# Performance work log

Measured on AMD Instinct MI355X. Metric: run time of the kernel, lower is better.

The kernel has to match this reference:

```python
import jax, jax.numpy as jnp
import numpy as np

HIDDEN = 64
NUM_LAYERS = 6
BN_EPS = 1e-5


def setup_inputs() -> dict:
    key = jax.random.key(0)
    N, M = 1024, 1024
    num_nodes = N + M
    ks = jax.random.split(key, 12)
    x = jax.random.normal(ks[0], (num_nodes, 2), dtype=jnp.float32)
    # complete bipartite edges: (a, N+b) for all a in [0,N), b in [0,M), row-major so view(N,M) is meaningful
    row = jnp.repeat(jnp.arange(N, dtype=jnp.int64), M)
    col = N + jnp.tile(jnp.arange(M, dtype=jnp.int64), N)
    edge_index = jnp.stack([row, col], axis=0)
    s = 1.0 / np.sqrt(HIDDEN)
    return {
        "x": x,
        "edge_index": edge_index,
        "in_w": jax.random.normal(ks[1], (2, HIDDEN), jnp.float32) * 0.5,
        "in_b": jnp.zeros((HIDDEN,), jnp.float32),
        "conv_w": jax.random.normal(ks[2], (NUM_LAYERS, HIDDEN, HIDDEN), jnp.float32) * s,
        "conv_b": jnp.zeros((NUM_LAYERS, HIDDEN), jnp.float32),
        "bn_gamma": jnp.ones((NUM_LAYERS, HIDDEN), jnp.float32),
        "bn_beta": jnp.zeros((NUM_LAYERS, HIDDEN), jnp.float32),
        "out_w": jax.random.normal(ks[3], (2 * HIDDEN, 1), jnp.float32) * s,
        "out_b": jnp.zeros((1,), jnp.float32),
        "N": N,
        "M": M,
    }


def reference(x, edge_index, in_w, in_b, conv_w, conv_b, bn_gamma, bn_beta, out_w, out_b, N, M):
    num_nodes = x.shape[0]
    # GCN normalization with added self-loops (PyG GCNConv defaults)
    loops = jnp.arange(num_nodes, dtype=edge_index.dtype)
    row = jnp.concatenate([edge_index[0], loops])
    col = jnp.concatenate([edge_index[1], loops])
    deg = jax.ops.segment_sum(jnp.ones_like(col, dtype=x.dtype), col, num_segments=num_nodes)
    dinv = jnp.where(deg > 0, jax.lax.rsqrt(deg), 0.0)
    norm = dinv[row] * dinv[col]  # [E+num_nodes]

    h = jax.nn.relu(x @ in_w + in_b)
    for i in range(NUM_LAYERS):
        h_res = h
        hw = h @ conv_w[i]
        agg = jax.ops.segment_sum(hw[row] * norm[:, None], col, num_segments=num_nodes)
        h = agg + conv_b[i]
        # BatchNorm1d in training mode: batch stats, biased variance
        mu = h.mean(axis=0)
        var = ((h - mu) ** 2).mean(axis=0)
        h = (h - mu) * jax.lax.rsqrt(var + BN_EPS) * bn_gamma[i] + bn_beta[i]
        h = jax.nn.relu(h)
        if i > 0 and i % 2 == 1:
            h = h + h_res

    ef = jnp.concatenate([h[edge_index[0]], h[edge_index[1]]], axis=1)  # [E, 2H]
    scores = (ef @ out_w + out_b)[:, 0]
    return scores.reshape(N, M)
```

## Files before the change

kernel.cpp:

```cpp
#include <hip/hip_runtime.h>


#define NBLK 64
#define MAGIC 0x13572468u

__device__ __forceinline__ float relu_(float x) { return x > 0.f ? x : 0.f; }

#define AT_LOAD(p)    __hip_atomic_load((p), __ATOMIC_RELAXED, __HIP_MEMORY_SCOPE_AGENT)
#define AT_STORE(p,v) __hip_atomic_store((p), (v), __ATOMIC_RELAXED, __HIP_MEMORY_SCOPE_AGENT)
#define AT_ADD(p,v)   __hip_atomic_fetch_add((p), (v), __ATOMIC_RELAXED, __HIP_MEMORY_SCOPE_AGENT)

#define PART_OFF  256
#define UV_OFF    12544
#define FLAG_OFF  14592

__global__ __launch_bounds__(256, 1) void k_fused(
    const float* __restrict__ x,
    const float* __restrict__ in_w, const float* __restrict__ in_b,
    const float* __restrict__ conv_w,
    const float* __restrict__ bn_g, const float* __restrict__ bn_b,
    const float* __restrict__ out_w,
    unsigned int* __restrict__ ws)
{
    __shared__ float Wl[2][4096];
    __shared__ float hl[32 * 68];
    __shared__ float sredS[4 * 64], sredQ[4 * 64];
    __shared__ float stat[256];
    __shared__ float pcoef[64], scoef[64];
    __shared__ float g_lds[384], b_lds[384];
    __shared__ float ow_lds[128];

    const int t = threadIdx.x, b = blockIdx.x;
    const int nl = t >> 3;
    const int fi = t & 7;
    const int f0 = fi * 8;
    const int node = b * 32 + nl;
    const bool isA = b < 32;
    float* part = (float*)(ws + PART_OFF);
    float* uv   = (float*)(ws + UV_OFF);

    {
        const float4* src = (const float4*)conv_w;
        float4* dst = (float4*)Wl[0];
        dst[t]       = src[t];
        dst[t + 256] = src[t + 256];
        dst[t + 512] = src[t + 512];
        dst[t + 768] = src[t + 768];
        for (int i = t; i < 384; i += 256) { g_lds[i] = bn_g[i]; b_lds[i] = bn_b[i]; }
        if (t < 128) ow_lds[t] = out_w[t];
    }

    if (b == 0) {
        for (int i = t; i < 192; i += 256) AT_STORE(ws + i, 0u);
        for (int i = t; i < 12288; i += 256) AT_STORE((unsigned*)part + i, 0u);
        asm volatile("s_waitcnt vmcnt(0)" ::: "memory");
        __syncthreads();
        if (t == 0) AT_STORE(ws + FLAG_OFF, MAGIC);
    }

    {
        float x0 = x[node * 2], x1 = x[node * 2 + 1];
#pragma unroll
        for (int j = 0; j < 8; j++) {
            int f = f0 + j;
            hl[nl * 68 + f] = relu_(fmaf(x0, in_w[f], fmaf(x1, in_w[64 + f], in_b[f])));
        }
    }
    __syncthreads();

    for (int layer = 0; layer < 6; layer++) {
        const float* Wb = Wl[layer & 1];
        float acc[8];
#pragma unroll
        for (int j = 0; j < 8; j++) acc[j] = 0.f;

#pragma unroll 4
        for (int k = 0; k < 64; k += 4) {
            float4 hh = *(const float4*)&hl[nl * 68 + k];
            float hv[4] = {hh.x, hh.y, hh.z, hh.w};
#pragma unroll
            for (int j = 0; j < 4; j++) {
                const float* wr = Wb + (k + j) * 64 + f0;
                float4 w0 = *(const float4*)wr;
                float4 w1 = *(const float4*)(wr + 4);
                float wv[8] = {w0.x, w0.y, w0.z, w0.w, w1.x, w1.y, w1.z, w1.w};
#pragma unroll
                for (int q = 0; q < 8; q++) acc[q] = fmaf(hv[j], wv[q], acc[q]);
            }
        }

        {
            float sv[8], qv[8];
#pragma unroll
            for (int j = 0; j < 8; j++) { sv[j] = acc[j]; qv[j] = acc[j] * acc[j]; }
#pragma unroll
            for (int m = 8; m < 64; m <<= 1) {
#pragma unroll
                for (int j = 0; j < 8; j++) {
                    sv[j] += __shfl_xor(sv[j], m);
                    qv[j] += __shfl_xor(qv[j], m);
                }
            }
            int w = t >> 6, lane = t & 63;
            if (lane < 8) {
#pragma unroll
                for (int j = 0; j < 8; j++) {
                    sredS[w * 64 + lane * 8 + j] = sv[j];
                    sredQ[w * 64 + lane * 8 + j] = qv[j];
                }
            }
        }
        if (layer == 0) {
            __syncthreads();
            if (t == 0) while (AT_LOAD(ws + FLAG_OFF) != MAGIC) {}
        }
        __syncthreads();

        if (t < 64) {
            float S = sredS[t] + sredS[64 + t] + sredS[128 + t] + sredS[192 + t];
            float Q = sredQ[t] + sredQ[64 + t] + sredQ[128 + t] + sredQ[192 + t];
            float* base = part + layer * 2048 + (b & 7) * 256 + (isA ? 0 : 128);
            AT_ADD(base + t, S);
            AT_ADD(base + 64 + t, Q);
        }

        asm volatile("s_waitcnt vmcnt(0)" ::: "memory");
        __syncthreads();
        if (t == 0) AT_ADD(ws + layer * 32, 1u);

        float4 pf0, pf1, pf2, pf3;
        if (layer < 5) {
            const float4* src = (const float4*)(conv_w + (layer + 1) * 4096);
            pf0 = src[t];
            pf1 = src[t + 256];
            pf2 = src[t + 512];
            pf3 = src[t + 768];
        }

        if (t == 0) {
            const unsigned int* c = ws + layer * 32;
            for (;;) {
                unsigned a0 = AT_LOAD(c);
                unsigned a1 = AT_LOAD(c);
                unsigned a2 = AT_LOAD(c);
                unsigned a3 = AT_LOAD(c);
                if (a0 >= NBLK) break;
                if (a1 >= NBLK) break;
                if (a2 >= NBLK) break;
                if (a3 >= NBLK) break;
            }
        }
        __syncthreads();

        {
            int item = t;
            const float* p = part + layer * 2048 + item;
            float s = 0.f;
#pragma unroll
            for (int r = 0; r < 8; r++) s += AT_LOAD(p + r * 256);
            stat[item] = s;
        }

        if (layer < 5) {
            float4* dst = (float4*)Wl[(layer + 1) & 1];
            dst[t]       = pf0;
            dst[t + 256] = pf1;
            dst[t + 512] = pf2;
            dst[t + 768] = pf3;
        }
        __syncthreads();

        if (t < 64) {
            float SA = stat[t], QA = stat[64 + t], SB = stat[128 + t], QB = stat[192 + t];
            const float c1 = 9.75609756097561e-4f;
            const float c2 = 3.1234752377721214e-2f;
            float sumAgg = SA + c1 * SB + 1024.f * c2 * SA;
            float sumSq  = QA + c1 * c1 * QB + 2.f * c1 * c2 * SA * SB
                         + 1024.f * c2 * c2 * SA * SA;
            float meanAgg = sumAgg * (1.f / 2048.f);
            float var = sumSq * (1.f / 2048.f) - meanAgg * meanAgg;
            float rstd = rsqrtf(var + 1e-5f);
            float scale = rstd * g_lds[layer * 64 + t];
            float bt = b_lds[layer * 64 + t];
            if (isA) { pcoef[t] = scale;      scoef[t] = bt - meanAgg * scale; }
            else     { pcoef[t] = c1 * scale; scoef[t] = bt + (c2 * SA - meanAgg) * scale; }
        }
        __syncthreads();

        float vals[8];
#pragma unroll
        for (int j = 0; j < 8; j++)
            vals[j] = relu_(fmaf(acc[j], pcoef[f0 + j], scoef[f0 + j]));
        if (layer == 1 || layer == 3 || layer == 5) {
#pragma unroll
            for (int j = 0; j < 8; j++) vals[j] += hl[nl * 68 + f0 + j];
        }

        if (layer < 5) {
#pragma unroll
            for (int j = 0; j < 8; j++) hl[nl * 68 + f0 + j] = vals[j];
            __syncthreads();
        } else {
            const float* w = ow_lds + (isA ? 0 : 64) + f0;
            float d = 0.f;
#pragma unroll
            for (int j = 0; j < 8; j++) d = fmaf(vals[j], w[j], d);
            d += __shfl_xor(d, 1);
            d += __shfl_xor(d, 2);
            d += __shfl_xor(d, 4);
            if (fi == 0) AT_STORE(uv + node, d);
        }
    }
}

__global__ __launch_bounds__(256) void k_out(const float* __restrict__ uv,
                                             const float* __restrict__ out_b,
                                             float* __restrict__ out) {
    const int a = blockIdx.x;
    const int t = threadIdx.x;
    float ua = uv[a] + out_b[0];
    float4 vv = ((const float4*)(uv + 1024))[t];
    ((float4*)(out + a * 1024))[t] =
        make_float4(ua + vv.x, ua + vv.y, ua + vv.z, ua + vv.w);
}

extern "C" void kernel_launch(void* const* d_in, const int* in_sizes, int n_in,
                              void* d_out, int out_size, void* d_ws, size_t ws_size,
                              hipStream_t stream) {
    const float* x      = (const float*)d_in[0];
    const float* in_w   = (const float*)d_in[2];
    const float* in_b   = (const float*)d_in[3];
    const float* conv_w = (const float*)d_in[4];
    const float* bn_g   = (const float*)d_in[6];
    const float* bn_b   = (const float*)d_in[7];
    const float* out_w  = (const float*)d_in[8];
    const float* out_b  = (const float*)d_in[9];
    float* out = (float*)d_out;

    unsigned int* ws = (unsigned int*)d_ws;
    const float* uv = (const float*)(ws + UV_OFF);

    k_fused<<<NBLK, 256, 0, stream>>>(x, in_w, in_b, conv_w, bn_g, bn_b,
                                      out_w, ws);
    k_out<<<1024, 256, 0, stream>>>(uv, out_b, out);
}
```

Before: 113.8 us.

## Halve fused kernel grid to 32 blocks with two nodes per thread

Result: no change. 115.7 us (+1.7%).

```diff
diff --git a/kernel.cpp b/kernel.cpp
--- a/kernel.cpp
+++ b/kernel.cpp
@@ -1,7 +1,7 @@
 #include <hip/hip_runtime.h>
 
 
-#define NBLK 64
+#define NBLK 32
 #define MAGIC 0x13572468u
 
 __device__ __forceinline__ float relu_(float x) { return x > 0.f ? x : 0.f; }
@@ -11,8 +11,8 @@
 #define AT_ADD(p,v)   __hip_atomic_fetch_add((p), (v), __ATOMIC_RELAXED, __HIP_MEMORY_SCOPE_AGENT)
 
 #define PART_OFF  256
-#define UV_OFF    12544
-#define FLAG_OFF  14592
+#define UV_OFF    6400
+#define FLAG_OFF  8448
 
 __global__ __launch_bounds__(256, 1) void k_fused(
     const float* __restrict__ x,
@@ -23,7 +23,7 @@
     unsigned int* __restrict__ ws)
 {
     __shared__ float Wl[2][4096];
-    __shared__ float hl[32 * 68];
+    __shared__ float hl[64 * 68];
     __shared__ float sredS[4 * 64], sredQ[4 * 64];
     __shared__ float stat[256];
     __shared__ float pcoef[64], scoef[64];
@@ -31,11 +31,12 @@
     __shared__ float ow_lds[128];
 
     const int t = threadIdx.x, b = blockIdx.x;
-    const int nl = t >> 3;
+    const int p  = t >> 3;
     const int fi = t & 7;
     const int f0 = fi * 8;
-    const int node = b * 32 + nl;
-    const bool isA = b < 32;
+    const int r0 = p, r1 = p + 32;
+    const int node0 = b * 64 + p, node1 = node0 + 32;
+    const bool isA = b < 16;
     float* part = (float*)(ws + PART_OFF);
     float* uv   = (float*)(ws + UV_OFF);
 
@@ -51,83 +52,26 @@
     }
 
     if (b == 0) {
-        for (int i = t; i < 192; i += 256) AT_STORE(ws + i, 0u);
-        for (int i = t; i < 12288; i += 256) AT_STORE((unsigned*)part + i, 0u);
+        for (int i = t; i < 6400; i += 256) AT_STORE(ws + i, 0u);
         asm volatile("s_waitcnt vmcnt(0)" ::: "memory");
         __syncthreads();
         if (t == 0) AT_STORE(ws + FLAG_OFF, MAGIC);
     }
 
     {
-        float x0 = x[node * 2], x1 = x[node * 2 + 1];
+        float x0 = x[node0 * 2], x1 = x[node0 * 2 + 1];
+        float y0 = x[node1 * 2], y1 = x[node1 * 2 + 1];
 #pragma unroll
         for (int j = 0; j < 8; j++) {
             int f = f0 + j;
-            hl[nl * 68 + f] = relu_(fmaf(x0, in_w[f], fmaf(x1, in_w[64 + f], in_b[f])));
+            float wa = in_w[f], wb = in_w[64 + f], bb = in_b[f];
+            hl[r0 * 68 + f] = relu_(fmaf(x0, wa, fmaf(x1, wb, bb)));
+            hl[r1 * 68 + f] = relu_(fmaf(y0, wa, fmaf(y1, wb, bb)));
         }
     }
     __syncthreads();
 
     for (int layer = 0; layer < 6; layer++) {
-        const float* Wb = Wl[layer & 1];
-        float acc[8];
-#pragma unroll
-        for (int j = 0; j < 8; j++) acc[j] = 0.f;
-
-#pragma unroll 4
-        for (int k = 0; k < 64; k += 4) {
-            float4 hh = *(const float4*)&hl[nl * 68 + k];
-            float hv[4] = {hh.x, hh.y, hh.z, hh.w};
-#pragma unroll
-            for (int j = 0; j < 4; j++) {
-                const float* wr = Wb + (k + j) * 64 + f0;
-                float4 w0 = *(const float4*)wr;
-                float4 w1 = *(const float4*)(wr + 4);
-                float wv[8] = {w0.x, w0.y, w0.z, w0.w, w1.x, w1.y, w1.z, w1.w};
-#pragma unroll
-                for (int q = 0; q < 8; q++) acc[q] = fmaf(hv[j], wv[q], acc[q]);
-            }
-        }
-
-        {
-            float sv[8], qv[8];
-#pragma unroll
-            for (int j = 0; j < 8; j++) { sv[j] = acc[j]; qv[j] = acc[j] * acc[j]; }
-#pragma unroll
-            for (int m = 8; m < 64; m <<= 1) {
-#pragma unroll
-                for (int j = 0; j < 8; j++) {
-                    sv[j] += __shfl_xor(sv[j], m);
-                    qv[j] += __shfl_xor(qv[j], m);
-                }
-            }
-            int w = t >> 6, lane = t & 63;
-            if (lane < 8) {
-#pragma unroll
-                for (int j = 0; j < 8; j++) {
-                    sredS[w * 64 + lane * 8 + j] = sv[j];
-                    sredQ[w * 64 + lane * 8 + j] = qv[j];
-                }
-            }
-        }
-        if (layer == 0) {
-            __syncthreads();
-            if (t == 0) while (AT_LOAD(ws + FLAG_OFF) != MAGIC) {}
-        }
-        __syncthreads();
-
-        if (t < 64) {
-            float S = sredS[t] + sredS[64 + t] + sredS[128 + t] + sredS[192 + t];
-            float Q = sredQ[t] + sredQ[64 + t] + sredQ[128 + t] + sredQ[192 + t];
-            float* base = part + layer * 2048 + (b & 7) * 256 + (isA ? 0 : 128);
-            AT_ADD(base + t, S);
-            AT_ADD(base + 64 + t, Q);
-        }
-
-        asm volatile("s_waitcnt vmcnt(0)" ::: "memory");
-        __syncthreads();
-        if (t == 0) AT_ADD(ws + layer * 32, 1u);
-
         float4 pf0, pf1, pf2, pf3;
         if (layer < 5) {
             const float4* src = (const float4*)(conv_w + (layer + 1) * 4096);
@@ -137,28 +81,29 @@
             pf3 = src[t + 768];
         }
 
-        if (t == 0) {
-            const unsigned int* c = ws + layer * 32;
-            for (;;) {
-                unsigned a0 = AT_LOAD(c);
-                unsigned a1 = AT_LOAD(c);
-                unsigned a2 = AT_LOAD(c);
-                unsigned a3 = AT_LOAD(c);
-                if (a0 >= NBLK) break;
-                if (a1 >= NBLK) break;
-                if (a2 >= NBLK) break;
-                if (a3 >= NBLK) break;
-            }
-        }
-        __syncthreads();
-
-        {
-            int item = t;
-            const float* p = part + layer * 2048 + item;
-            float s = 0.f;
-#pragma unroll
-            for (int r = 0; r < 8; r++) s += AT_LOAD(p + r * 256);
-            stat[item] = s;
+        const float* Wb = Wl[layer & 1];
+        float acc0[8], acc1[8];
+#pragma unroll
+        for (int j = 0; j < 8; j++) { acc0[j] = 0.f; acc1[j] = 0.f; }
+
+#pragma unroll 4
+        for (int k = 0; k < 64; k += 4) {
+            float4 ha = *(const float4*)&hl[r0 * 68 + k];
+            float4 hb = *(const float4*)&hl[r1 * 68 + k];
+            float hav[4] = {ha.x, ha.y, ha.z, ha.w};
+            float hbv[4] = {hb.x, hb.y, hb.z, hb.w};
+#pragma unroll
+            for (int j = 0; j < 4; j++) {
+                const float* wr = Wb + (k + j) * 64 + f0;
+                float4 w0 = *(const float4*)wr;
+                float4 w1 = *(const float4*)(wr + 4);
+                float wv[8] = {w0.x, w0.y, w0.z, w0.w, w1.x, w1.y, w1.z, w1.w};
+#pragma unroll
+                for (int q = 0; q < 8; q++) {
+                    acc0[q] = fmaf(hav[j], wv[q], acc0[q]);
+                    acc1[q] = fmaf(hbv[j], wv[q], acc1[q]);
+                }
+            }
         }
 
         if (layer < 5) {
@@ -167,6 +112,66 @@
             dst[t + 256] = pf1;
             dst[t + 512] = pf2;
             dst[t + 768] = pf3;
+        }
+
+        {
+            float sv[8], qv[8];
+#pragma unroll
+            for (int j = 0; j < 8; j++) {
+                sv[j] = acc0[j] + acc1[j];
+                qv[j] = fmaf(acc0[j], acc0[j], acc1[j] * acc1[j]);
+            }
+#pragma unroll
+            for (int m = 8; m < 64; m <<= 1) {
+#pragma unroll
+                for (int j = 0; j < 8; j++) {
+                    sv[j] += __shfl_xor(sv[j], m);
+                    qv[j] += __shfl_xor(qv[j], m);
+                }
+            }
+            int w = t >> 6, lane = t & 63;
+            if (lane < 8) {
+#pragma unroll
+                for (int j = 0; j < 8; j++) {
+                    sredS[w * 64 + lane * 8 + j] = sv[j];
+                    sredQ[w * 64 + lane * 8 + j] = qv[j];
+                }
+            }
+        }
+        if (layer == 0) {
+            __syncthreads();
+            if (t == 0) while (AT_LOAD(ws + FLAG_OFF) != MAGIC) {}
+        }
+        __syncthreads();
+
+        if (t < 64) {
+            float S = sredS[t] + sredS[64 + t] + sredS[128 + t] + sredS[192 + t];
+            float Q = sredQ[t] + sredQ[64 + t] + sredQ[128 + t] + sredQ[192 + t];
+            float* base = part + layer * 1024 + (b & 3) * 256 + (isA ? 0 : 128);
+            AT_ADD(base + t, S);
+            AT_ADD(base + 64 + t, Q);
+            asm volatile("s_waitcnt vmcnt(0)" ::: "memory");
+            if (t == 0) {
+                AT_ADD(ws + layer * 32, 1u);
+                const unsigned int* c = ws + layer * 32;
+                for (;;) {
+                    unsigned a0 = AT_LOAD(c);
+                    unsigned a1 = AT_LOAD(c);
+                    unsigned a2 = AT_LOAD(c);
+                    unsigned a3 = AT_LOAD(c);
+                    if (a0 >= NBLK) break;
+                    if (a1 >= NBLK) break;
+                    if (a2 >= NBLK) break;
+                    if (a3 >= NBLK) break;
+                }
+            }
+        }
+        __syncthreads();
+
+        {
+            const float* pp = part + layer * 1024 + t;
+            float s = AT_LOAD(pp) + AT_LOAD(pp + 256) + AT_LOAD(pp + 512) + AT_LOAD(pp + 768);
+            stat[t] = s;
         }
         __syncthreads();
 
@@ -187,28 +192,44 @@
         }
         __syncthreads();
 
-        float vals[8];
-#pragma unroll
-        for (int j = 0; j < 8; j++)
-            vals[j] = relu_(fmaf(acc[j], pcoef[f0 + j], scoef[f0 + j]));
+        float v0[8], v1[8];
+#pragma unroll
+        for (int j = 0; j < 8; j++) {
+            float pc = pcoef[f0 + j], sc = scoef[f0 + j];
+            v0[j] = relu_(fmaf(acc0[j], pc, sc));
+            v1[j] = relu_(fmaf(acc1[j], pc, sc));
+        }
         if (layer == 1 || layer == 3 || layer == 5) {
 #pragma unroll
-            for (int j = 0; j < 8; j++) vals[j] += hl[nl * 68 + f0 + j];
+            for (int j = 0; j < 8; j++) {
+                v0[j] += hl[r0 * 68 + f0 + j];
+                v1[j] += hl[r1 * 68 + f0 + j];
+            }
         }
 
         if (layer < 5) {
-#pragma unroll
-            for (int j = 0; j < 8; j++) hl[nl * 68 + f0 + j] = vals[j];
+            __syncthreads();
+#pragma unroll
+            for (int j = 0; j < 8; j++) {
+                hl[r0 * 68 + f0 + j] = v0[j];
+                hl[r1 * 68 + f0 + j] = v1[j];
+            }
             __syncthreads();
         } else {
             const float* w = ow_lds + (isA ? 0 : 64) + f0;
-            float d = 0.f;
-#pragma unroll
-            for (int j = 0; j < 8; j++) d = fmaf(vals[j], w[j], d);
-            d += __shfl_xor(d, 1);
-            d += __shfl_xor(d, 2);
-            d += __shfl_xor(d, 4);
-            if (fi == 0) AT_STORE(uv + node, d);
+            float d0 = 0.f, d1 = 0.f;
+#pragma unroll
+            for (int j = 0; j < 8; j++) {
+                d0 = fmaf(v0[j], w[j], d0);
+                d1 = fmaf(v1[j], w[j], d1);
+            }
+            d0 += __shfl_xor(d0, 1); d1 += __shfl_xor(d1, 1);
+            d0 += __shfl_xor(d0, 2); d1 += __shfl_xor(d1, 2);
+            d0 += __shfl_xor(d0, 4); d1 += __shfl_xor(d1, 4);
+            if (fi == 0) {
+                AT_STORE(uv + node0, d0);
+                AT_STORE(uv + node1, d1);
+            }
         }
     }
 }
```

## Replace counter barrier with fixed-point 64-bit atomics carrying embedded arrival counts

Applied to the files above, without the earlier changes.

New measurement: 126.4 us. 1.11x slower.

```diff
diff --git a/kernel.cpp b/kernel.cpp
--- a/kernel.cpp
+++ b/kernel.cpp
@@ -3,16 +3,18 @@
 
 #define NBLK 64
 #define MAGIC 0x13572468u
+#define FIXSCALE 1048576.0f
+#define BIAS (1ll << 40)
 
 __device__ __forceinline__ float relu_(float x) { return x > 0.f ? x : 0.f; }
 
 #define AT_LOAD(p)    __hip_atomic_load((p), __ATOMIC_RELAXED, __HIP_MEMORY_SCOPE_AGENT)
 #define AT_STORE(p,v) __hip_atomic_store((p), (v), __ATOMIC_RELAXED, __HIP_MEMORY_SCOPE_AGENT)
-#define AT_ADD(p,v)   __hip_atomic_fetch_add((p), (v), __ATOMIC_RELAXED, __HIP_MEMORY_SCOPE_AGENT)
-
-#define PART_OFF  256
-#define UV_OFF    12544
-#define FLAG_OFF  14592
+#define AT_ADD64(p,v) __hip_atomic_fetch_add((p), (v), __ATOMIC_RELAXED, __HIP_MEMORY_SCOPE_AGENT)
+#define AT_LOAD64(p)  __hip_atomic_load((p), __ATOMIC_RELAXED, __HIP_MEMORY_SCOPE_AGENT)
+
+#define ACC_OFF   64
+#define UV_OFF    6208
 
 __global__ __launch_bounds__(256, 1) void k_fused(
     const float* __restrict__ x,
@@ -25,7 +27,7 @@
     __shared__ float Wl[2][4096];
     __shared__ float hl[32 * 68];
     __shared__ float sredS[4 * 64], sredQ[4 * 64];
-    __shared__ float stat[256];
+    __shared__ float redp[128][2];
     __shared__ float pcoef[64], scoef[64];
     __shared__ float g_lds[384], b_lds[384];
     __shared__ float ow_lds[128];
@@ -36,8 +38,8 @@
     const int f0 = fi * 8;
     const int node = b * 32 + nl;
     const bool isA = b < 32;
-    float* part = (float*)(ws + PART_OFF);
-    float* uv   = (float*)(ws + UV_OFF);
+    unsigned long long* acc64 = (unsigned long long*)(ws + ACC_OFF);
+    float* uv = (float*)(ws + UV_OFF);
 
     {
         const float4* src = (const float4*)conv_w;
@@ -51,11 +53,10 @@
     }
 
     if (b == 0) {
-        for (int i = t; i < 192; i += 256) AT_STORE(ws + i, 0u);
-        for (int i = t; i < 12288; i += 256) AT_STORE((unsigned*)part + i, 0u);
+        for (int i = t; i < 6144; i += 256) AT_STORE(ws + ACC_OFF + i, 0u);
         asm volatile("s_waitcnt vmcnt(0)" ::: "memory");
         __syncthreads();
-        if (t == 0) AT_STORE(ws + FLAG_OFF, MAGIC);
+        if (t == 0) AT_STORE(ws, MAGIC);
     }
 
     {
@@ -69,65 +70,6 @@
     __syncthreads();
 
     for (int layer = 0; layer < 6; layer++) {
-        const float* Wb = Wl[layer & 1];
-        float acc[8];
-#pragma unroll
-        for (int j = 0; j < 8; j++) acc[j] = 0.f;
-
-#pragma unroll 4
-        for (int k = 0; k < 64; k += 4) {
-            float4 hh = *(const float4*)&hl[nl * 68 + k];
-            float hv[4] = {hh.x, hh.y, hh.z, hh.w};
-#pragma unroll
-            for (int j = 0; j < 4; j++) {
-                const float* wr = Wb + (k + j) * 64 + f0;
-                float4 w0 = *(const float4*)wr;
-                float4 w1 = *(const float4*)(wr + 4);
-                float wv[8] = {w0.x, w0.y, w0.z, w0.w, w1.x, w1.y, w1.z, w1.w};
-#pragma unroll
-                for (int q = 0; q < 8; q++) acc[q] = fmaf(hv[j], wv[q], acc[q]);
-            }
-        }
-
-        {
-            float sv[8], qv[8];
-#pragma unroll
-            for (int j = 0; j < 8; j++) { sv[j] = acc[j]; qv[j] = acc[j] * acc[j]; }
-#pragma unroll
-            for (int m = 8; m < 64; m <<= 1) {
-#pragma unroll
-                for (int j = 0; j < 8; j++) {
-                    sv[j] += __shfl_xor(sv[j], m);
-                    qv[j] += __shfl_xor(qv[j], m);
-                }
-            }
-            int w = t >> 6, lane = t & 63;
-            if (lane < 8) {
-#pragma unroll
-                for (int j = 0; j < 8; j++) {
-                    sredS[w * 64 + lane * 8 + j] = sv[j];
-                    sredQ[w * 64 + lane * 8 + j] = qv[j];
-                }
-            }
-        }
-        if (layer == 0) {
-            __syncthreads();
-            if (t == 0) while (AT_LOAD(ws + FLAG_OFF) != MAGIC) {}
-        }
-        __syncthreads();
-
-        if (t < 64) {
-            float S = sredS[t] + sredS[64 + t] + sredS[128 + t] + sredS[192 + t];
-            float Q = sredQ[t] + sredQ[64 + t] + sredQ[128 + t] + sredQ[192 + t];
-            float* base = part + layer * 2048 + (b & 7) * 256 + (isA ? 0 : 128);
-            AT_ADD(base + t, S);
-            AT_ADD(base + 64 + t, Q);
-        }
-
-        asm volatile("s_waitcnt vmcnt(0)" ::: "memory");
-        __syncthreads();
-        if (t == 0) AT_ADD(ws + layer * 32, 1u);
-
         float4 pf0, pf1, pf2, pf3;
         if (layer < 5) {
             const float4* src = (const float4*)(conv_w + (layer + 1) * 4096);
@@ -137,28 +79,24 @@
             pf3 = src[t + 768];
         }
 
-        if (t == 0) {
-            const unsigned int* c = ws + layer * 32;
-            for (;;) {
-                unsigned a0 = AT_LOAD(c);
-                unsigned a1 = AT_LOAD(c);
-                unsigned a2 = AT_LOAD(c);
-                unsigned a3 = AT_LOAD(c);
-                if (a0 >= NBLK) break;
-                if (a1 >= NBLK) break;
-                if (a2 >= NBLK) break;
-                if (a3 >= NBLK) break;
-            }
-        }
-        __syncthreads();
-
-        {
-            int item = t;
-            const float* p = part + layer * 2048 + item;
-            float s = 0.f;
-#pragma unroll
-            for (int r = 0; r < 8; r++) s += AT_LOAD(p + r * 256);
-            stat[item] = s;
+        const float* Wb = Wl[layer & 1];
+        float acc[8];
+#pragma unroll
+        for (int j = 0; j < 8; j++) acc[j] = 0.f;
+
+#pragma unroll 4
+        for (int k = 0; k < 64; k += 4) {
+            float4 hh = *(const float4*)&hl[nl * 68 + k];
+            float hv[4] = {hh.x, hh.y, hh.z, hh.w};
+#pragma unroll
+            for (int j = 0; j < 4; j++) {
+                const float* wr = Wb + (k + j) * 64 + f0;
+                float4 w0 = *(const float4*)wr;
+                float4 w1 = *(const float4*)(wr + 4);
+                float wv[8] = {w0.x, w0.y, w0.z, w0.w, w1.x, w1.y, w1.z, w1.w};
+#pragma unroll
+                for (int q = 0; q < 8; q++) acc[q] = fmaf(hv[j], wv[q], acc[q]);
+            }
         }
 
         if (layer < 5) {
@@ -168,10 +106,64 @@
             dst[t + 512] = pf2;
             dst[t + 768] = pf3;
         }
+
+        {
+            float sv[8], qv[8];
+#pragma unroll
+            for (int j = 0; j < 8; j++) { sv[j] = acc[j]; qv[j] = acc[j] * acc[j]; }
+#pragma unroll
+            for (int m = 8; m < 64; m <<= 1) {
+#pragma unroll
+                for (int j = 0; j < 8; j++) {
+                    sv[j] += __shfl_xor(sv[j], m);
+                    qv[j] += __shfl_xor(qv[j], m);
+                }
+            }
+            int w = t >> 6, lane = t & 63;
+            if (lane < 8) {
+#pragma unroll
+                for (int j = 0; j < 8; j++) {
+                    sredS[w * 64 + lane * 8 + j] = sv[j];
+                    sredQ[w * 64 + lane * 8 + j] = qv[j];
+                }
+            }
+        }
+        if (layer == 0) {
+            __syncthreads();
+            if (t == 0) while (AT_LOAD(ws) != MAGIC) {}
+        }
+        __syncthreads();
+
+        if (t < 128) {
+            float val = (t < 64)
+                ? sredS[t] + sredS[64 + t] + sredS[128 + t] + sredS[192 + t]
+                : sredQ[t - 64] + sredQ[t] + sredQ[t + 64] + sredQ[t + 128];
+            long long fx = (long long)llrintf(val * FIXSCALE);
+            unsigned long long contrib =
+                (1ull << 48) + (unsigned long long)(fx + BIAS);
+            int rep = (isA ? 0 : 2) + (b & 1);
+            AT_ADD64(acc64 + (size_t)layer * 512 + t * 4 + rep, contrib);
+        }
+
+        {
+            int item = t >> 1, side = t & 1;
+            unsigned long long* base =
+                acc64 + (size_t)layer * 512 + item * 4 + side * 2;
+            unsigned long long w0, w1;
+            for (;;) {
+                w0 = AT_LOAD64(base);
+                w1 = AT_LOAD64(base + 1);
+                if ((w0 >> 48) == 16 && (w1 >> 48) == 16) break;
+            }
+            long long s0 = (long long)(w0 & 0xFFFFFFFFFFFFull) - 16ll * BIAS;
+            long long s1 = (long long)(w1 & 0xFFFFFFFFFFFFull) - 16ll * BIAS;
+            redp[item][side] = (float)(s0 + s1) * (1.0f / FIXSCALE);
+        }
         __syncthreads();
 
         if (t < 64) {
-            float SA = stat[t], QA = stat[64 + t], SB = stat[128 + t], QB = stat[192 + t];
+            float SA = redp[t][0],      SB = redp[t][1];
+            float QA = redp[64 + t][0], QB = redp[64 + t][1];
             const float c1 = 9.75609756097561e-4f;
             const float c2 = 3.1234752377721214e-2f;
             float sumAgg = SA + c1 * SB + 1024.f * c2 * SA;
```

## Replace block-wide barriers with per-wave grid sync and shuffle-broadcast BN coefficients

Applied to the files above, without the earlier changes.

Result: slower. 117.9 us (+3.6%).

```diff
diff --git a/kernel.cpp b/kernel.cpp
--- a/kernel.cpp
+++ b/kernel.cpp
@@ -10,9 +10,9 @@
 #define AT_STORE(p,v) __hip_atomic_store((p), (v), __ATOMIC_RELAXED, __HIP_MEMORY_SCOPE_AGENT)
 #define AT_ADD(p,v)   __hip_atomic_fetch_add((p), (v), __ATOMIC_RELAXED, __HIP_MEMORY_SCOPE_AGENT)
 
-#define PART_OFF  256
-#define UV_OFF    12544
-#define FLAG_OFF  14592
+#define CNT_OFF   64
+#define PART_OFF  1024
+#define UV_OFF    7168
 
 __global__ __launch_bounds__(256, 1) void k_fused(
     const float* __restrict__ x,
@@ -25,8 +25,6 @@
     __shared__ float Wl[2][4096];
     __shared__ float hl[32 * 68];
     __shared__ float sredS[4 * 64], sredQ[4 * 64];
-    __shared__ float stat[256];
-    __shared__ float pcoef[64], scoef[64];
     __shared__ float g_lds[384], b_lds[384];
     __shared__ float ow_lds[128];
 
@@ -34,6 +32,8 @@
     const int nl = t >> 3;
     const int fi = t & 7;
     const int f0 = fi * 8;
+    const int lane = t & 63;
+    const int wv = t >> 6;
     const int node = b * 32 + nl;
     const bool isA = b < 32;
     float* part = (float*)(ws + PART_OFF);
@@ -51,11 +51,10 @@
     }
 
     if (b == 0) {
-        for (int i = t; i < 192; i += 256) AT_STORE(ws + i, 0u);
-        for (int i = t; i < 12288; i += 256) AT_STORE((unsigned*)part + i, 0u);
+        for (int i = t; i < 7104; i += 256) AT_STORE(ws + CNT_OFF + i, 0u);
         asm volatile("s_waitcnt vmcnt(0)" ::: "memory");
         __syncthreads();
-        if (t == 0) AT_STORE(ws + FLAG_OFF, MAGIC);
+        if (t == 0) AT_STORE(ws, MAGIC);
     }
 
     {
@@ -69,65 +68,6 @@
     __syncthreads();
 
     for (int layer = 0; layer < 6; layer++) {
-        const float* Wb = Wl[layer & 1];
-        float acc[8];
-#pragma unroll
-        for (int j = 0; j < 8; j++) acc[j] = 0.f;
-
-#pragma unroll 4
-        for (int k = 0; k < 64; k += 4) {
-            float4 hh = *(const float4*)&hl[nl * 68 + k];
-            float hv[4] = {hh.x, hh.y, hh.z, hh.w};
-#pragma unroll
-            for (int j = 0; j < 4; j++) {
-                const float* wr = Wb + (k + j) * 64 + f0;
-                float4 w0 = *(const float4*)wr;
-                float4 w1 = *(const float4*)(wr + 4);
-                float wv[8] = {w0.x, w0.y, w0.z, w0.w, w1.x, w1.y, w1.z, w1.w};
-#pragma unroll
-                for (int q = 0; q < 8; q++) acc[q] = fmaf(hv[j], wv[q], acc[q]);
-            }
-        }
-
-        {
-            float sv[8], qv[8];
-#pragma unroll
-            for (int j = 0; j < 8; j++) { sv[j] = acc[j]; qv[j] = acc[j] * acc[j]; }
-#pragma unroll
-            for (int m = 8; m < 64; m <<= 1) {
-#pragma unroll
-                for (int j = 0; j < 8; j++) {
-                    sv[j] += __shfl_xor(sv[j], m);
-                    qv[j] += __shfl_xor(qv[j], m);
-                }
-            }
-            int w = t >> 6, lane = t & 63;
-            if (lane < 8) {
-#pragma unroll
-                for (int j = 0; j < 8; j++) {
-                    sredS[w * 64 + lane * 8 + j] = sv[j];
-                    sredQ[w * 64 + lane * 8 + j] = qv[j];
-                }
-            }
-        }
-        if (layer == 0) {
-            __syncthreads();
-            if (t == 0) while (AT_LOAD(ws + FLAG_OFF) != MAGIC) {}
-        }
-        __syncthreads();
-
-        if (t < 64) {
-            float S = sredS[t] + sredS[64 + t] + sredS[128 + t] + sredS[192 + t];
-            float Q = sredQ[t] + sredQ[64 + t] + sredQ[128 + t] + sredQ[192 + t];
-            float* base = part + layer * 2048 + (b & 7) * 256 + (isA ? 0 : 128);
-            AT_ADD(base + t, S);
-            AT_ADD(base + 64 + t, Q);
-        }
-
-        asm volatile("s_waitcnt vmcnt(0)" ::: "memory");
-        __syncthreads();
-        if (t == 0) AT_ADD(ws + layer * 32, 1u);
-
         float4 pf0, pf1, pf2, pf3;
         if (layer < 5) {
             const float4* src = (const float4*)(conv_w + (layer + 1) * 4096);
@@ -137,28 +77,24 @@
             pf3 = src[t + 768];
         }
 
-        if (t == 0) {
-            const unsigned int* c = ws + layer * 32;
-            for (;;) {
-                unsigned a0 = AT_LOAD(c);
-                unsigned a1 = AT_LOAD(c);
-                unsigned a2 = AT_LOAD(c);
-                unsigned a3 = AT_LOAD(c);
-                if (a0 >= NBLK) break;
-                if (a1 >= NBLK) break;
-                if (a2 >= NBLK) break;
-                if (a3 >= NBLK) break;
-            }
-        }
-        __syncthreads();
-
-        {
-            int item = t;
-            const float* p = part + layer * 2048 + item;
-            float s = 0.f;
-#pragma unroll
-            for (int r = 0; r < 8; r++) s += AT_LOAD(p + r * 256);
-            stat[item] = s;
+        const float* Wb = Wl[layer & 1];
+        float acc[8];
+#pragma unroll
+        for (int j = 0; j < 8; j++) acc[j] = 0.f;
+
+#pragma unroll 4
+        for (int k = 0; k < 64; k += 4) {
+            float4 hh = *(const float4*)&hl[nl * 68 + k];
+            float hv[4] = {hh.x, hh.y, hh.z, hh.w};
+#pragma unroll
+            for (int j = 0; j < 4; j++) {
+                const float* wr = Wb + (k + j) * 64 + f0;
+                float4 w0 = *(const float4*)wr;
+                float4 w1 = *(const float4*)(wr + 4);
+                float wv8[8] = {w0.x, w0.y, w0.z, w0.w, w1.x, w1.y, w1.z, w1.w};
+#pragma unroll
+                for (int q = 0; q < 8; q++) acc[q] = fmaf(hv[j], wv8[q], acc[q]);
+            }
         }
 
         if (layer < 5) {
@@ -168,10 +104,71 @@
             dst[t + 512] = pf2;
             dst[t + 768] = pf3;
         }
+
+        {
+            float sv[8], qv[8];
+#pragma unroll
+            for (int j = 0; j < 8; j++) { sv[j] = acc[j]; qv[j] = acc[j] * acc[j]; }
+#pragma unroll
+            for (int m = 8; m < 64; m <<= 1) {
+#pragma unroll
+                for (int j = 0; j < 8; j++) {
+                    sv[j] += __shfl_xor(sv[j], m);
+                    qv[j] += __shfl_xor(qv[j], m);
+                }
+            }
+            if (lane < 8) {
+#pragma unroll
+                for (int j = 0; j < 8; j++) {
+                    sredS[wv * 64 + lane * 8 + j] = sv[j];
+                    sredQ[wv * 64 + lane * 8 + j] = qv[j];
+                }
+            }
+        }
         __syncthreads();
 
-        if (t < 64) {
-            float SA = stat[t], QA = stat[64 + t], SB = stat[128 + t], QB = stat[192 + t];
+        if (layer == 0) {
+            if (lane == 0) while (AT_LOAD(ws) != MAGIC) {}
+        }
+
+        if (wv == 0) {
+            float S = sredS[lane] + sredS[64 + lane] + sredS[128 + lane] + sredS[192 + lane];
+            float Q = sredQ[lane] + sredQ[64 + lane] + sredQ[128 + lane] + sredQ[192 + lane];
+            float* base = part + layer * 1024 + (b & 3) * 256 + (isA ? 0 : 128);
+            AT_ADD(base + lane, S);
+            AT_ADD(base + 64 + lane, Q);
+            asm volatile("s_waitcnt vmcnt(0)" ::: "memory");
+            if (lane < 4) AT_ADD(ws + CNT_OFF + (layer * 4 + lane) * 32, 1u);
+        }
+
+        {
+            const unsigned int* c = ws + CNT_OFF + (layer * 4 + wv) * 32;
+            if (lane == 0) {
+                for (;;) {
+                    unsigned a0 = AT_LOAD(c);
+                    unsigned a1 = AT_LOAD(c);
+                    unsigned a2 = AT_LOAD(c);
+                    unsigned a3 = AT_LOAD(c);
+                    if (a0 >= NBLK) break;
+                    if (a1 >= NBLK) break;
+                    if (a2 >= NBLK) break;
+                    if (a3 >= NBLK) break;
+                }
+            }
+        }
+
+        float pc_f, sc_f;
+        {
+            const float* base = part + layer * 1024;
+            float SA = 0.f, QA = 0.f, SB = 0.f, QB = 0.f;
+#pragma unroll
+            for (int r = 0; r < 4; r++) {
+                const float* rb = base + r * 256;
+                SA += AT_LOAD(rb + lane);
+                QA += AT_LOAD(rb + 64 + lane);
+                SB += AT_LOAD(rb + 128 + lane);
+                QB += AT_LOAD(rb + 192 + lane);
+            }
             const float c1 = 9.75609756097561e-4f;
             const float c2 = 3.1234752377721214e-2f;
             float sumAgg = SA + c1 * SB + 1024.f * c2 * SA;
@@ -180,17 +177,19 @@
             float meanAgg = sumAgg * (1.f / 2048.f);
             float var = sumSq * (1.f / 2048.f) - meanAgg * meanAgg;
             float rstd = rsqrtf(var + 1e-5f);
-            float scale = rstd * g_lds[layer * 64 + t];
-            float bt = b_lds[layer * 64 + t];
-            if (isA) { pcoef[t] = scale;      scoef[t] = bt - meanAgg * scale; }
-            else     { pcoef[t] = c1 * scale; scoef[t] = bt + (c2 * SA - meanAgg) * scale; }
-        }
-        __syncthreads();
+            float scale = rstd * g_lds[layer * 64 + lane];
+            float bt = b_lds[layer * 64 + lane];
+            if (isA) { pc_f = scale;      sc_f = bt - meanAgg * scale; }
+            else     { pc_f = c1 * scale; sc_f = bt + (c2 * SA - meanAgg) * scale; }
+        }
 
         float vals[8];
 #pragma unroll
-        for (int j = 0; j < 8; j++)
-            vals[j] = relu_(fmaf(acc[j], pcoef[f0 + j], scoef[f0 + j]));
+        for (int j = 0; j < 8; j++) {
+            float pc = __shfl(pc_f, f0 + j);
+            float sc = __shfl(sc_f, f0 + j);
+            vals[j] = relu_(fmaf(acc[j], pc, sc));
+        }
         if (layer == 1 || layer == 3 || layer == 5) {
 #pragma unroll
             for (int j = 0; j < 8; j++) vals[j] += hl[nl * 68 + f0 + j];
```
